# Performance work log

Measured on AMD Instinct MI355X. Metric: run time of the kernel, lower is better.

Reference implementation:

```python
import jax, jax.numpy as jnp
import numpy as np

H = 16  # hidden size = time_slot(=32) / 2
G = 3 * H  # gate dim (r|z|n), torch gate order


def _gru_dir(x, Wi, Wh, bi, bh, reverse):
    """Single-direction GRU over time. x: [B,T,F]; Wi:[3H,F]; Wh:[3H,H]."""
    xp = jnp.einsum('btf,gf->btg', x, Wi) + bi  # [B,T,3H] input projections, all steps at once
    if reverse:
        xp = xp[:, ::-1]
    xp_t = jnp.swapaxes(xp, 0, 1)  # [T,B,3H]
    h0 = jnp.zeros((x.shape[0], H), x.dtype)

    def step(h, g_x):
        g_h = h @ Wh.T + bh  # [B,3H]
        r = jax.nn.sigmoid(g_x[:, :H] + g_h[:, :H])
        z = jax.nn.sigmoid(g_x[:, H:2 * H] + g_h[:, H:2 * H])
        n = jnp.tanh(g_x[:, 2 * H:] + r * g_h[:, 2 * H:])
        h_new = (1.0 - z) * n + z * h
        return h_new, h_new

    _, ys = jax.lax.scan(step, h0, xp_t)
    ys = jnp.swapaxes(ys, 0, 1)  # [B,T,H]
    if reverse:
        ys = ys[:, ::-1]
    return ys


def _bigru(x, Wi, Wh, bi, bh):
    """Bidirectional GRU layer; params indexed [dir(2), ...]."""
    fwd = _gru_dir(x, Wi[0], Wh[0], bi[0], bh[0], False)
    bwd = _gru_dir(x, Wi[1], Wh[1], bi[1], bh[1], True)
    return jnp.concatenate([fwd, bwd], axis=-1)  # [B,T,2H]


def setup_inputs() -> dict:
    key = jax.random.key(0)
    ks = jax.random.split(key, 12)
    B, T, F_IN, DEPTH, NCLS = 16384, 64, 3, 5, 4
    s = 0.25  # ~1/sqrt(H) torch init scale
    return {
        'x': jax.random.normal(ks[0], (B, T, F_IN), jnp.float32),
        # GRU1: 1 layer, 2 directions, input 3
        'Wi1': jax.random.normal(ks[1], (2, G, F_IN), jnp.float32) * s,
        'Wh1': jax.random.normal(ks[2], (2, G, H), jnp.float32) * s,
        'bi1': jax.random.normal(ks[3], (2, G), jnp.float32) * s,
        'bh1': jax.random.normal(ks[4], (2, G), jnp.float32) * s,
        # GRU5: 5 layers, 2 directions, input 2H=32 every layer
        'Wi5': jax.random.normal(ks[5], (DEPTH, 2, G, 2 * H), jnp.float32) * s,
        'Wh5': jax.random.normal(ks[6], (DEPTH, 2, G, H), jnp.float32) * s,
        'bi5': jax.random.normal(ks[7], (DEPTH, 2, G), jnp.float32) * s,
        'bh5': jax.random.normal(ks[8], (DEPTH, 2, G), jnp.float32) * s,
        # classifier Linear(2H -> num_class)
        'Wc': jax.random.normal(ks[9], (NCLS, 2 * H), jnp.float32) * s,
        'bc': jax.random.normal(ks[10], (NCLS,), jnp.float32) * s,
    }


def reference(x, Wi1, Wh1, bi1, bh1, Wi5, Wh5, bi5, bh5, Wc, bc):
    y = _bigru(x, Wi1, Wh1, bi1, bh1)  # [B,T,2H]
    for l in range(Wi5.shape[0]):  # 5 stacked bi-GRU layers
        y = _bigru(y, Wi5[l], Wh5[l], bi5[l], bh5[l])
    logits = jnp.einsum('btd,cd->btc', y, Wc) + bc  # [B,T,num_class]
    return jax.nn.softmax(logits, axis=2)
```

## Files before the change

### kernel.cpp

```cpp
#include <hip/hip_runtime.h>

#define T 64
#define F_IN 3
#define H 16
#define G 48
#define D2 32
#define DEPTH 5
#define NCLS 4

#define YST 32
#define YSB 2048
#define HZ_ZOFF 64

typedef _Float16 half8 __attribute__((ext_vector_type(8)));
typedef _Float16 half4v __attribute__((ext_vector_type(4)));
typedef float f32x4v __attribute__((ext_vector_type(4)));

__global__ __launch_bounds__(64, 3) void bigru_all(
    const float* __restrict__ x,
    const float* __restrict__ Wi1, const float* __restrict__ Wh1,
    const float* __restrict__ bi1, const float* __restrict__ bh1,
    const float* __restrict__ Wi5, const float* __restrict__ Wh5,
    const float* __restrict__ bi5, const float* __restrict__ bh5,
    const float* __restrict__ Wc,  const float* __restrict__ bc,
    float* __restrict__ out)
{
    __shared__ __align__(16) _Float16 yb[2 * YSB];
    __shared__ __align__(16) _Float16 hzb[80];

    const int lane = threadIdx.x;
    const int j15  = lane & 15;
    const int quad = lane >> 4;
    const int lb   = quad & 1;
    const int dir  = quad >> 1;
    const bool isf = (dir == 0);

    hzb[lane] = (_Float16)0.0f;
    if (lane < 16) hzb[64 + lane] = (_Float16)0.0f;

    const int  job_a  = j15 >> 2;
    const bool avalid = ((j15 >> 3) == 0) ? (quad < 2) : (quad >= 2);
    const _Float16* aptr = hzb + (avalid ? (job_a * 16 + (quad & 1) * 8) : HZ_ZOFF);

    const int ystep = isf ? YST : -YST;
    const f32x4v zC = {0.f, 0.f, 0.f, 0.f};

    float hj;

    {
        half8 whB[3];
        {
            const float* wsrc = Wh1 + ((quad < 2) ? 0 : G * H);
            #pragma unroll
            for (int g = 0; g < 3; ++g) {
                const float scale = (g == 2) ? -2.0f : 1.0f;
                const float* w = wsrc + (g * 16 + j15) * H + (quad & 1) * 8;
                half8 hv;
                #pragma unroll
                for (int i = 0; i < 8; ++i) hv[i] = (_Float16)(scale * w[i]);
                whB[g] = hv;
            }
        }
        float wi[3][F_IN];
        float bir[3], bhn2;
        {
            const float* Wi = Wi1 + dir * (G * F_IN);
            const float* bi = bi1 + dir * G;
            const float* bh = bh1 + dir * G;
            #pragma unroll
            for (int g = 0; g < 3; ++g) {
                const float scale = (g == 2) ? -2.0f : 1.0f;
                int row = g * H + j15;
                #pragma unroll
                for (int k = 0; k < F_IN; ++k) wi[g][k] = scale * Wi[row * F_IN + k];
                bir[g] = scale * bi[row] + ((g < 2) ? bh[row] : 0.0f);
            }
            bhn2 = -2.0f * bh[2 * H + j15];
        }
        const f32x4v cN = {bhn2, bhn2, bhn2, bhn2};
        hj = 0.0f;

        const float* xg = x + (size_t)blockIdx.x * (2 * T * F_IN) + (size_t)lb * (T * F_IN);
        _Float16* yw = yb + lb * YSB + (isf ? 0 : (T - 1)) * YST + dir * H + j15;

        #pragma unroll 4
        for (int s = 0; s < T; ++s) {
            int t = isf ? s : (T - 1 - s);
            const float* xp = xg + t * F_IN;
            float x0 = xp[0], x1 = xp[1], x2 = xp[2];
            float gxr = fmaf(wi[0][2], x2, fmaf(wi[0][1], x1, fmaf(wi[0][0], x0, bir[0])));
            float gxz = fmaf(wi[1][2], x2, fmaf(wi[1][1], x1, fmaf(wi[1][0], x0, bir[1])));
            float gxn = fmaf(wi[2][2], x2, fmaf(wi[2][1], x1, fmaf(wi[2][0], x0, bir[2])));
            half8 a = *(const half8*)aptr;
            f32x4v d0 = __builtin_amdgcn_mfma_f32_16x16x32_f16(a, whB[0], zC, 0, 0, 0);
            f32x4v d1 = __builtin_amdgcn_mfma_f32_16x16x32_f16(a, whB[1], zC, 0, 0, 0);
            f32x4v d2 = __builtin_amdgcn_mfma_f32_16x16x32_f16(a, whB[2], cN, 0, 0, 0);
            float av = gxr + d0[0];
            float bv = gxz + d1[0];
            float Er = __expf(fminf(40.f, -av));
            float rg = __builtin_amdgcn_rcpf(1.0f + Er);
            float c2 = fmaf(rg, d2[0], gxn);
            float Ez = __expf(fminf(40.f, -bv));
            float Ec = __expf(fminf(44.f, c2));
            float num = fmaf(hj - Ez, Ec, hj + Ez);
            float den = (1.0f + Ec) * (1.0f + Ez);
            float hn = num * __builtin_amdgcn_rcpf(den);
            hj = hn;
            _Float16 hh = (_Float16)hn;
            hzb[lane] = hh;
            *yw = hh;
            yw += ystep;
        }
    }

    #pragma unroll 1
    for (int l = 0; l < DEPTH; ++l) {
        half8 bf[2][3];
        #pragma unroll
        for (int d = 0; d < 2; ++d) {
            #pragma unroll
            for (int g = 0; g < 3; ++g) {
                const float scale = (g == 2) ? -2.0f : 1.0f;
                const float* w = Wi5 + ((size_t)(l * 2 + d) * G + g * 16 + j15) * D2 + quad * 8;
                half8 hv;
                #pragma unroll
                for (int i = 0; i < 8; ++i) hv[i] = (_Float16)(scale * w[i]);
                bf[d][g] = hv;
            }
        }
        half8 whB[3];
        {
            const float* wsrc = Wh5 + (size_t)(l * 2) * G * H + ((quad < 2) ? 0 : G * H);
            #pragma unroll
            for (int g = 0; g < 3; ++g) {
                const float scale = (g == 2) ? -2.0f : 1.0f;
                const float* w = wsrc + (g * 16 + j15) * H + (quad & 1) * 8;
                half8 hv;
                #pragma unroll
                for (int i = 0; i < 8; ++i) hv[i] = (_Float16)(scale * w[i]);
                whB[g] = hv;
            }
        }
        float bib0, bib1, bib2, bhn2;
        {
            const float* biL = bi5 + (l * 2 + dir) * G;
            const float* bhL = bh5 + (l * 2 + dir) * G;
            bib0 = biL[j15]         + bhL[j15];
            bib1 = biL[H + j15]     + bhL[H + j15];
            bib2 = -2.0f * biL[2 * H + j15];
            bhn2 = -2.0f * bhL[2 * H + j15];
        }
        const f32x4v cR  = {bib0, bib0, bib0, bib0};
        const f32x4v cZ  = {bib1, bib1, bib1, bib1};
        const f32x4v cNx = {bib2, bib2, bib2, bib2};
        const f32x4v cN  = {bhn2, bhn2, bhn2, bhn2};

        hj = 0.0f;
        hzb[lane] = (_Float16)0.0f;

        const int lb_a = (j15 >> 2) & 1;
        const int tl_a = j15 & 3;

        unsigned int ypk[16];

        #pragma unroll
        for (int c = 0; c < 8; ++c) {
            const int tf = 4 * c;
            const int tb = T - 4 - 4 * c;
            const int row = (j15 < 8) ? (tf + tl_a) : (tb + tl_a);
            half8 ax = *(const half8*)(yb + lb_a * YSB + row * YST + quad * 8);
            f32x4v c0f = __builtin_amdgcn_mfma_f32_16x16x32_f16(ax, bf[0][0], cR, 0, 0, 0);
            f32x4v c1f = __builtin_amdgcn_mfma_f32_16x16x32_f16(ax, bf[0][1], cZ, 0, 0, 0);
            f32x4v c2f = __builtin_amdgcn_mfma_f32_16x16x32_f16(ax, bf[0][2], cNx, 0, 0, 0);
            f32x4v c0b = __builtin_amdgcn_mfma_f32_16x16x32_f16(ax, bf[1][0], cR, 0, 0, 0);
            f32x4v c1b = __builtin_amdgcn_mfma_f32_16x16x32_f16(ax, bf[1][1], cZ, 0, 0, 0);
            f32x4v c2b = __builtin_amdgcn_mfma_f32_16x16x32_f16(ax, bf[1][2], cNx, 0, 0, 0);

            #pragma unroll
            for (int s = 0; s < 4; ++s) {
                float gx0 = isf ? c0f[s] : c0b[3 - s];
                float gx1 = isf ? c1f[s] : c1b[3 - s];
                float gx2 = isf ? c2f[s] : c2b[3 - s];
                half8 a = *(const half8*)aptr;
                f32x4v d0 = __builtin_amdgcn_mfma_f32_16x16x32_f16(a, whB[0], zC, 0, 0, 0);
                f32x4v d1 = __builtin_amdgcn_mfma_f32_16x16x32_f16(a, whB[1], zC, 0, 0, 0);
                f32x4v d2 = __builtin_amdgcn_mfma_f32_16x16x32_f16(a, whB[2], cN, 0, 0, 0);
                float av = gx0 + d0[0];
                float bv = gx1 + d1[0];
                float Er = __expf(fminf(40.f, -av));
                float rg = __builtin_amdgcn_rcpf(1.0f + Er);
                float c2 = fmaf(rg, d2[0], gx2);
                float Ez = __expf(fminf(40.f, -bv));
                float Ec = __expf(fminf(44.f, c2));
                float num = fmaf(hj - Ez, Ec, hj + Ez);
                float den = (1.0f + Ec) * (1.0f + Ez);
                float hn = num * __builtin_amdgcn_rcpf(den);
                hj = hn;
                _Float16 hh = (_Float16)hn;
                hzb[lane] = hh;
                unsigned int hb16 = (unsigned int)__builtin_bit_cast(unsigned short, hh);
                if (s & 1) ypk[2 * c + (s >> 1)] |= hb16 << 16;
                else       ypk[2 * c + (s >> 1)]  = hb16;
            }
        }

        {
            _Float16* yw = yb + lb * YSB + (isf ? 32 : 31) * YST + dir * H + j15;
            #pragma unroll 1
            for (int c = 8; c < 16; ++c) {
                const int tf = 4 * c;
                const int tb = T - 4 - 4 * c;
                const int row = (j15 < 8) ? (tf + tl_a) : (tb + tl_a);
                half8 ax = *(const half8*)(yb + lb_a * YSB + row * YST + quad * 8);
                f32x4v c0f = __builtin_amdgcn_mfma_f32_16x16x32_f16(ax, bf[0][0], cR, 0, 0, 0);
                f32x4v c1f = __builtin_amdgcn_mfma_f32_16x16x32_f16(ax, bf[0][1], cZ, 0, 0, 0);
                f32x4v c2f = __builtin_amdgcn_mfma_f32_16x16x32_f16(ax, bf[0][2], cNx, 0, 0, 0);
                f32x4v c0b = __builtin_amdgcn_mfma_f32_16x16x32_f16(ax, bf[1][0], cR, 0, 0, 0);
                f32x4v c1b = __builtin_amdgcn_mfma_f32_16x16x32_f16(ax, bf[1][1], cZ, 0, 0, 0);
                f32x4v c2b = __builtin_amdgcn_mfma_f32_16x16x32_f16(ax, bf[1][2], cNx, 0, 0, 0);

                #pragma unroll
                for (int s = 0; s < 4; ++s) {
                    float gx0 = isf ? c0f[s] : c0b[3 - s];
                    float gx1 = isf ? c1f[s] : c1b[3 - s];
                    float gx2 = isf ? c2f[s] : c2b[3 - s];
                    half8 a = *(const half8*)aptr;
                    f32x4v d0 = __builtin_amdgcn_mfma_f32_16x16x32_f16(a, whB[0], zC, 0, 0, 0);
                    f32x4v d1 = __builtin_amdgcn_mfma_f32_16x16x32_f16(a, whB[1], zC, 0, 0, 0);
                    f32x4v d2 = __builtin_amdgcn_mfma_f32_16x16x32_f16(a, whB[2], cN, 0, 0, 0);
                    float av = gx0 + d0[0];
                    float bv = gx1 + d1[0];
                    float Er = __expf(fminf(40.f, -av));
                    float rg = __builtin_amdgcn_rcpf(1.0f + Er);
                    float c2 = fmaf(rg, d2[0], gx2);
                    float Ez = __expf(fminf(40.f, -bv));
                    float Ec = __expf(fminf(44.f, c2));
                    float num = fmaf(hj - Ez, Ec, hj + Ez);
                    float den = (1.0f + Ec) * (1.0f + Ez);
                    float hn = num * __builtin_amdgcn_rcpf(den);
                    hj = hn;
                    _Float16 hh = (_Float16)hn;
                    hzb[lane] = hh;
                    *yw = hh;
                    yw += ystep;
                }
            }
        }

        {
            _Float16* yw = yb + lb * YSB + (isf ? 0 : (T - 1)) * YST + dir * H + j15;
            #pragma unroll
            for (int i = 0; i < 16; ++i) {
                unsigned int v = ypk[i];
                *yw = __builtin_bit_cast(_Float16, (unsigned short)(v & 0xffffu));
                yw += ystep;
                *yw = __builtin_bit_cast(_Float16, (unsigned short)(v >> 16));
                yw += ystep;
            }
        }
    }

    #pragma unroll
    for (int i = 0; i < 2; ++i) {
        int idx = lane + i * 64;
        int bb  = idx >> 6;
        int t   = idx & 63;
        const _Float16* yrow = yb + bb * YSB + t * YST;
        float yv[D2];
        #pragma unroll
        for (int k8 = 0; k8 < 4; ++k8) {
            half8 v = *(const half8*)(yrow + k8 * 8);
            #pragma unroll
            for (int i8 = 0; i8 < 8; ++i8) yv[k8 * 8 + i8] = (float)v[i8];
        }
        float lg[NCLS];
        #pragma unroll
        for (int c = 0; c < NCLS; ++c) {
            const float* wc = Wc + c * D2;
            float acc = bc[c];
            #pragma unroll
            for (int k = 0; k < D2; ++k) acc = fmaf(wc[k], yv[k], acc);
            lg[c] = acc;
        }
        float m = fmaxf(fmaxf(lg[0], lg[1]), fmaxf(lg[2], lg[3]));
        float e0 = __expf(lg[0] - m), e1 = __expf(lg[1] - m);
        float e2 = __expf(lg[2] - m), e3 = __expf(lg[3] - m);
        float inv = __builtin_amdgcn_rcpf(e0 + e1 + e2 + e3);
        size_t bglob = (size_t)blockIdx.x * 2 + bb;
        float4 o;
        o.x = e0 * inv; o.y = e1 * inv; o.z = e2 * inv; o.w = e3 * inv;
        ((float4*)out)[bglob * T + t] = o;
    }
}

extern "C" void kernel_launch(void* const* d_in, const int* in_sizes, int n_in,
                              void* d_out, int out_size, void* d_ws, size_t ws_size,
                              hipStream_t stream) {
    const float* x   = (const float*)d_in[0];
    const float* Wi1 = (const float*)d_in[1];
    const float* Wh1 = (const float*)d_in[2];
    const float* bi1 = (const float*)d_in[3];
    const float* bh1 = (const float*)d_in[4];
    const float* Wi5 = (const float*)d_in[5];
    const float* Wh5 = (const float*)d_in[6];
    const float* bi5 = (const float*)d_in[7];
    const float* bh5 = (const float*)d_in[8];
    const float* Wc  = (const float*)d_in[9];
    const float* bc  = (const float*)d_in[10];
    float* out = (float*)d_out;

    const int B = in_sizes[0] / (T * F_IN);
    dim3 grid(B / 2), block(64);
    hipLaunchKernelGGL(bigru_all, grid, block, 0, stream,
                       x, Wi1, Wh1, bi1, bh1, Wi5, Wh5, bi5, bh5, Wc, bc, out);
}
```

Baseline: 364.0 us.

## Fold log2e into weights for exp2 and block-diagonalize input projection MFMAs

Scales all gate weights and biases by log2(e) at load time, so the recurrence calls the hardware exp2 directly and skips the multiply that __expf performs internally. The input projection is also restructured. Instead of six MFMAs per 4-step chunk (fwd and bwd weights both applied to the full 32-wide input, then a per-direction select), it uses a block-diagonal A operand built from split lo/hi K halves with zero padding, and issues three accumulate pairs that produce each direction's gates directly. This adds a second LDS read per chunk and chains dependent MFMAs in exchange for removing the select logic and lowering register pressure. Clamp constants are rescaled to match.

```diff
diff --git a/kernel.cpp b/kernel.cpp
--- a/kernel.cpp
+++ b/kernel.cpp
@@ -7,14 +7,17 @@
 #define D2 32
 #define DEPTH 5
 #define NCLS 4
+#define L2E 1.44269504f
 
 #define YST 32
 #define YSB 2048
 #define HZ_ZOFF 64
 
 typedef _Float16 half8 __attribute__((ext_vector_type(8)));
-typedef _Float16 half4v __attribute__((ext_vector_type(4)));
 typedef float f32x4v __attribute__((ext_vector_type(4)));
+
+__device__ __forceinline__ float fexp2(float x) { return __builtin_amdgcn_exp2f(x); }
+__device__ __forceinline__ float frcp(float x)  { return __builtin_amdgcn_rcpf(x); }
 
 __global__ __launch_bounds__(64, 3) void bigru_all(
     const float* __restrict__ x,
@@ -44,17 +47,19 @@
 
     const int ystep = isf ? YST : -YST;
     const f32x4v zC = {0.f, 0.f, 0.f, 0.f};
+    const int klo = (quad & 1) * 8;
+    const int bdir = (quad < 2) ? 0 : 1;
 
     float hj;
 
     {
         half8 whB[3];
         {
-            const float* wsrc = Wh1 + ((quad < 2) ? 0 : G * H);
+            const float* wsrc = Wh1 + bdir * (G * H);
             #pragma unroll
             for (int g = 0; g < 3; ++g) {
-                const float scale = (g == 2) ? -2.0f : 1.0f;
-                const float* w = wsrc + (g * 16 + j15) * H + (quad & 1) * 8;
+                const float scale = (g == 2) ? (-2.0f * L2E) : L2E;
+                const float* w = wsrc + (g * 16 + j15) * H + klo;
                 half8 hv;
                 #pragma unroll
                 for (int i = 0; i < 8; ++i) hv[i] = (_Float16)(scale * w[i]);
@@ -69,13 +74,13 @@
             const float* bh = bh1 + dir * G;
             #pragma unroll
             for (int g = 0; g < 3; ++g) {
-                const float scale = (g == 2) ? -2.0f : 1.0f;
+                const float scale = (g == 2) ? (-2.0f * L2E) : L2E;
                 int row = g * H + j15;
                 #pragma unroll
                 for (int k = 0; k < F_IN; ++k) wi[g][k] = scale * Wi[row * F_IN + k];
-                bir[g] = scale * bi[row] + ((g < 2) ? bh[row] : 0.0f);
-            }
-            bhn2 = -2.0f * bh[2 * H + j15];
+                bir[g] = scale * bi[row] + ((g < 2) ? (L2E * bh[row]) : 0.0f);
+            }
+            bhn2 = -2.0f * L2E * bh[2 * H + j15];
         }
         const f32x4v cN = {bhn2, bhn2, bhn2, bhn2};
         hj = 0.0f;
@@ -97,14 +102,14 @@
             f32x4v d2 = __builtin_amdgcn_mfma_f32_16x16x32_f16(a, whB[2], cN, 0, 0, 0);
             float av = gxr + d0[0];
             float bv = gxz + d1[0];
-            float Er = __expf(fminf(40.f, -av));
-            float rg = __builtin_amdgcn_rcpf(1.0f + Er);
+            float Er = fexp2(fminf(58.f, -av));
+            float rg = frcp(1.0f + Er);
             float c2 = fmaf(rg, d2[0], gxn);
-            float Ez = __expf(fminf(40.f, -bv));
-            float Ec = __expf(fminf(44.f, c2));
+            float Ez = fexp2(fminf(58.f, -bv));
+            float Ec = fexp2(fminf(63.f, c2));
             float num = fmaf(hj - Ez, Ec, hj + Ez);
             float den = (1.0f + Ec) * (1.0f + Ez);
-            float hn = num * __builtin_amdgcn_rcpf(den);
+            float hn = num * frcp(den);
             hj = hn;
             _Float16 hh = (_Float16)hn;
             hzb[lane] = hh;
@@ -115,26 +120,27 @@
 
     #pragma unroll 1
     for (int l = 0; l < DEPTH; ++l) {
-        half8 bf[2][3];
+        half8 bflo[3], bfhi[3];
         #pragma unroll
-        for (int d = 0; d < 2; ++d) {
+        for (int g = 0; g < 3; ++g) {
+            const float scale = (g == 2) ? (-2.0f * L2E) : L2E;
+            const float* w = Wi5 + ((size_t)(l * 2 + bdir) * G + g * 16 + j15) * D2;
+            half8 lo, hi;
+            #pragma unroll
+            for (int i = 0; i < 8; ++i) {
+                lo[i] = (_Float16)(scale * w[klo + i]);
+                hi[i] = (_Float16)(scale * w[16 + klo + i]);
+            }
+            bflo[g] = lo;
+            bfhi[g] = hi;
+        }
+        half8 whB[3];
+        {
+            const float* wsrc = Wh5 + ((size_t)(l * 2) + bdir) * G * H;
             #pragma unroll
             for (int g = 0; g < 3; ++g) {
-                const float scale = (g == 2) ? -2.0f : 1.0f;
-                const float* w = Wi5 + ((size_t)(l * 2 + d) * G + g * 16 + j15) * D2 + quad * 8;
-                half8 hv;
-                #pragma unroll
-                for (int i = 0; i < 8; ++i) hv[i] = (_Float16)(scale * w[i]);
-                bf[d][g] = hv;
-            }
-        }
-        half8 whB[3];
-        {
-            const float* wsrc = Wh5 + (size_t)(l * 2) * G * H + ((quad < 2) ? 0 : G * H);
-            #pragma unroll
-            for (int g = 0; g < 3; ++g) {
-                const float scale = (g == 2) ? -2.0f : 1.0f;
-                const float* w = wsrc + (g * 16 + j15) * H + (quad & 1) * 8;
+                const float scale = (g == 2) ? (-2.0f * L2E) : L2E;
+                const float* w = wsrc + (g * 16 + j15) * H + klo;
                 half8 hv;
                 #pragma unroll
                 for (int i = 0; i < 8; ++i) hv[i] = (_Float16)(scale * w[i]);
@@ -145,10 +151,10 @@
         {
             const float* biL = bi5 + (l * 2 + dir) * G;
             const float* bhL = bh5 + (l * 2 + dir) * G;
-            bib0 = biL[j15]         + bhL[j15];
-            bib1 = biL[H + j15]     + bhL[H + j15];
-            bib2 = -2.0f * biL[2 * H + j15];
-            bhn2 = -2.0f * bhL[2 * H + j15];
+            bib0 = L2E * (biL[j15]     + bhL[j15]);
+            bib1 = L2E * (biL[H + j15] + bhL[H + j15]);
+            bib2 = -2.0f * L2E * biL[2 * H + j15];
+            bhn2 = -2.0f * L2E * bhL[2 * H + j15];
         }
         const f32x4v cR  = {bib0, bib0, bib0, bib0};
         const f32x4v cZ  = {bib1, bib1, bib1, bib1};
@@ -158,43 +164,42 @@
         hj = 0.0f;
         hzb[lane] = (_Float16)0.0f;
 
-        const int lb_a = (j15 >> 2) & 1;
-        const int tl_a = j15 & 3;
+        const bool fsel = (j15 < 8);
+        const int  lb_a = (j15 >> 2) & 1;
+        const int  tl_a = j15 & 3;
+        const bool axv  = fsel ? (quad < 2) : (quad >= 2);
 
         unsigned int ypk[16];
 
         #pragma unroll
         for (int c = 0; c < 8; ++c) {
-            const int tf = 4 * c;
-            const int tb = T - 4 - 4 * c;
-            const int row = (j15 < 8) ? (tf + tl_a) : (tb + tl_a);
-            half8 ax = *(const half8*)(yb + lb_a * YSB + row * YST + quad * 8);
-            f32x4v c0f = __builtin_amdgcn_mfma_f32_16x16x32_f16(ax, bf[0][0], cR, 0, 0, 0);
-            f32x4v c1f = __builtin_amdgcn_mfma_f32_16x16x32_f16(ax, bf[0][1], cZ, 0, 0, 0);
-            f32x4v c2f = __builtin_amdgcn_mfma_f32_16x16x32_f16(ax, bf[0][2], cNx, 0, 0, 0);
-            f32x4v c0b = __builtin_amdgcn_mfma_f32_16x16x32_f16(ax, bf[1][0], cR, 0, 0, 0);
-            f32x4v c1b = __builtin_amdgcn_mfma_f32_16x16x32_f16(ax, bf[1][1], cZ, 0, 0, 0);
-            f32x4v c2b = __builtin_amdgcn_mfma_f32_16x16x32_f16(ax, bf[1][2], cNx, 0, 0, 0);
+            const int trow = fsel ? (4 * c + tl_a) : (T - 1 - 4 * c - tl_a);
+            const _Float16* abase = yb + lb_a * YSB + trow * YST;
+            half8 alo = *(const half8*)(axv ? (abase + klo)      : (hzb + HZ_ZOFF));
+            half8 ahi = *(const half8*)(axv ? (abase + 16 + klo) : (hzb + HZ_ZOFF));
+            f32x4v c0 = __builtin_amdgcn_mfma_f32_16x16x32_f16(alo, bflo[0], cR, 0, 0, 0);
+            f32x4v c1 = __builtin_amdgcn_mfma_f32_16x16x32_f16(alo, bflo[1], cZ, 0, 0, 0);
+            f32x4v c2g = __builtin_amdgcn_mfma_f32_16x16x32_f16(alo, bflo[2], cNx, 0, 0, 0);
+            c0  = __builtin_amdgcn_mfma_f32_16x16x32_f16(ahi, bfhi[0], c0, 0, 0, 0);
+            c1  = __builtin_amdgcn_mfma_f32_16x16x32_f16(ahi, bfhi[1], c1, 0, 0, 0);
+            c2g = __builtin_amdgcn_mfma_f32_16x16x32_f16(ahi, bfhi[2], c2g, 0, 0, 0);
 
             #pragma unroll
             for (int s = 0; s < 4; ++s) {
-                float gx0 = isf ? c0f[s] : c0b[3 - s];
-                float gx1 = isf ? c1f[s] : c1b[3 - s];
-                float gx2 = isf ? c2f[s] : c2b[3 - s];
                 half8 a = *(const half8*)aptr;
                 f32x4v d0 = __builtin_amdgcn_mfma_f32_16x16x32_f16(a, whB[0], zC, 0, 0, 0);
                 f32x4v d1 = __builtin_amdgcn_mfma_f32_16x16x32_f16(a, whB[1], zC, 0, 0, 0);
                 f32x4v d2 = __builtin_amdgcn_mfma_f32_16x16x32_f16(a, whB[2], cN, 0, 0, 0);
-                float av = gx0 + d0[0];
-                float bv = gx1 + d1[0];
-                float Er = __expf(fminf(40.f, -av));
-                float rg = __builtin_amdgcn_rcpf(1.0f + Er);
-                float c2 = fmaf(rg, d2[0], gx2);
-                float Ez = __expf(fminf(40.f, -bv));
-                float Ec = __expf(fminf(44.f, c2));
+                float av = c0[s] + d0[0];
+                float bv = c1[s] + d1[0];
+                float Er = fexp2(fminf(58.f, -av));
+                float rg = frcp(1.0f + Er);
+                float cc = fmaf(rg, d2[0], c2g[s]);
+                float Ez = fexp2(fminf(58.f, -bv));
+                float Ec = fexp2(fminf(63.f, cc));
                 float num = fmaf(hj - Ez, Ec, hj + Ez);
                 float den = (1.0f + Ec) * (1.0f + Ez);
-                float hn = num * __builtin_amdgcn_rcpf(den);
+                float hn = num * frcp(den);
                 hj = hn;
                 _Float16 hh = (_Float16)hn;
                 hzb[lane] = hh;
@@ -208,36 +213,33 @@
             _Float16* yw = yb + lb * YSB + (isf ? 32 : 31) * YST + dir * H + j15;
             #pragma unroll 1
             for (int c = 8; c < 16; ++c) {
-                const int tf = 4 * c;
-                const int tb = T - 4 - 4 * c;
-                const int row = (j15 < 8) ? (tf + tl_a) : (tb + tl_a);
-                half8 ax = *(const half8*)(yb + lb_a * YSB + row * YST + quad * 8);
-                f32x4v c0f = __builtin_amdgcn_mfma_f32_16x16x32_f16(ax, bf[0][0], cR, 0, 0, 0);
-                f32x4v c1f = __builtin_amdgcn_mfma_f32_16x16x32_f16(ax, bf[0][1], cZ, 0, 0, 0);
-                f32x4v c2f = __builtin_amdgcn_mfma_f32_16x16x32_f16(ax, bf[0][2], cNx, 0, 0, 0);
-                f32x4v c0b = __builtin_amdgcn_mfma_f32_16x16x32_f16(ax, bf[1][0], cR, 0, 0, 0);
-                f32x4v c1b = __builtin_amdgcn_mfma_f32_16x16x32_f16(ax, bf[1][1], cZ, 0, 0, 0);
-                f32x4v c2b = __builtin_amdgcn_mfma_f32_16x16x32_f16(ax, bf[1][2], cNx, 0, 0, 0);
+                const int trow = fsel ? (4 * c + tl_a) : (T - 1 - 4 * c - tl_a);
+                const _Float16* abase = yb + lb_a * YSB + trow * YST;
+                half8 alo = *(const half8*)(axv ? (abase + klo)      : (hzb + HZ_ZOFF));
+                half8 ahi = *(const half8*)(axv ? (abase + 16 + klo) : (hzb + HZ_ZOFF));
+                f32x4v c0 = __builtin_amdgcn_mfma_f32_16x16x32_f16(alo, bflo[0], cR, 0, 0, 0);
+                f32x4v c1 = __builtin_amdgcn_mfma_f32_16x16x32_f16(alo, bflo[1], cZ, 0, 0, 0);
+                f32x4v c2g = __builtin_amdgcn_mfma_f32_16x16x32_f16(alo, bflo[2], cNx, 0, 0, 0);
+                c0  = __builtin_amdgcn_mfma_f32_16x16x32_f16(ahi, bfhi[0], c0, 0, 0, 0);
+                c1  = __builtin_amdgcn_mfma_f32_16x16x32_f16(ahi, bfhi[1], c1, 0, 0, 0);
+                c2g = __builtin_amdgcn_mfma_f32_16x16x32_f16(ahi, bfhi[2], c2g, 0, 0, 0);
 
                 #pragma unroll
                 for (int s = 0; s < 4; ++s) {
-                    float gx0 = isf ? c0f[s] : c0b[3 - s];
-                    float gx1 = isf ? c1f[s] : c1b[3 - s];
-                    float gx2 = isf ? c2f[s] : c2b[3 - s];
                     half8 a = *(const half8*)aptr;
                     f32x4v d0 = __builtin_amdgcn_mfma_f32_16x16x32_f16(a, whB[0], zC, 0, 0, 0);
                     f32x4v d1 = __builtin_amdgcn_mfma_f32_16x16x32_f16(a, whB[1], zC, 0, 0, 0);
                     f32x4v d2 = __builtin_amdgcn_mfma_f32_16x16x32_f16(a, whB[2], cN, 0, 0, 0);
-                    float av = gx0 + d0[0];
-                    float bv = gx1 + d1[0];
-                    float Er = __expf(fminf(40.f, -av));
-                    float rg = __builtin_amdgcn_rcpf(1.0f + Er);
-                    float c2 = fmaf(rg, d2[0], gx2);
-                    float Ez = __expf(fminf(40.f, -bv));
-                    float Ec = __expf(fminf(44.f, c2));
+                    float av = c0[s] + d0[0];
+                    float bv = c1[s] + d1[0];
+                    float Er = fexp2(fminf(58.f, -av));
+                    float rg = frcp(1.0f + Er);
+                    float cc = fmaf(rg, d2[0], c2g[s]);
+                    float Ez = fexp2(fminf(58.f, -bv));
+                    float Ec = fexp2(fminf(63.f, cc));
                     float num = fmaf(hj - Ez, Ec, hj + Ez);
                     float den = (1.0f + Ec) * (1.0f + Ez);
-                    float hn = num * __builtin_amdgcn_rcpf(den);
+                    float hn = num * frcp(den);
                     hj = hn;
                     _Float16 hh = (_Float16)hn;
                     hzb[lane] = hh;
@@ -285,7 +287,7 @@
         float m = fmaxf(fmaxf(lg[0], lg[1]), fmaxf(lg[2], lg[3]));
         float e0 = __expf(lg[0] - m), e1 = __expf(lg[1] - m);
         float e2 = __expf(lg[2] - m), e3 = __expf(lg[3] - m);
-        float inv = __builtin_amdgcn_rcpf(e0 + e1 + e2 + e3);
+        float inv = frcp(e0 + e1 + e2 + e3);
         size_t bglob = (size_t)blockIdx.x * 2 + bb;
         float4 o;
         o.x = e0 * inv; o.y = e1 * inv; o.z = e2 * inv; o.w = e3 * inv;
```

Result: faster. 349.6 us (-4.0%).
